# Kernel optimization log

Hardware: AMD Instinct MI355X
Metric: run time of the kernel (lower is better)

The kernel has to match this reference:

```python
import jax, jax.numpy as jnp
import numpy as np

TEMP = 0.05
BIG = 1e6


def _mlp(z, W1, b1, W2, b2, W3, b3, W4, b4, W5, b5):
    h = jax.nn.selu(z @ W1 + b1)
    h = jax.nn.selu(h @ W2 + b2)
    h = jax.nn.selu(h @ W3 + b3)
    h = jax.nn.selu(h @ W4 + b4)
    return h @ W5 + b5


def _cdist(a, b):
    # Euclidean distance via ||a||^2 + ||b||^2 - 2 a.b (clamped for fp safety)
    d2 = (jnp.sum(a * a, axis=1)[:, None]
          + jnp.sum(b * b, axis=1)[None, :]
          - 2.0 * (a @ b.T))
    return jnp.sqrt(jnp.maximum(d2, 0.0))


def _compute_drift(x, y_pos, y_neg):
    N, N_pos = x.shape[0], y_pos.shape[0]
    dist_pos = _cdist(x, y_pos)                      # [N, N_pos]
    dist_neg = _cdist(x, y_neg)                      # [N, N_neg]
    if N == y_neg.shape[0]:
        dist_neg = dist_neg + jnp.eye(N, dtype=x.dtype) * BIG
    logit = jnp.concatenate([-dist_pos / TEMP, -dist_neg / TEMP], axis=1)
    for _ in range(5):  # Sinkhorn: alternating row / column normalization
        logit = logit - jax.nn.logsumexp(logit, axis=-1, keepdims=True)
        logit = logit - jax.nn.logsumexp(logit, axis=-2, keepdims=True)
    A = jnp.exp(logit)
    A_pos, A_neg = A[:, :N_pos], A[:, N_pos:]
    W_pos = A_pos * jnp.sum(A_neg, axis=1, keepdims=True)
    W_neg = A_neg * jnp.sum(A_pos, axis=1, keepdims=True)
    return W_pos @ y_pos - W_neg @ y_neg             # [N, D]


def _forward(pos, z, W1, b1, W2, b2, W3, b3, W4, b4, W5, b5):
    gen = _mlp(z, W1, b1, W2, b2, W3, b3, W4, b4, W5, b5)
    V = _compute_drift(gen, pos, gen)                # computed under no_grad
    target = jax.lax.stop_gradient(gen + V)
    return jnp.sum((gen - target) ** 2, axis=-1)      # per-sample loss [N]


def setup_inputs() -> dict:
    key = jax.random.key(0)
    ks = jax.random.split(key, 8)
    N, D, ND, H = 8192, 256, 128, 1024
    def w(k, fan_in, fan_out):
        return jax.random.normal(k, (fan_in, fan_out), jnp.float32) / np.float32(np.sqrt(fan_in))
    return {
        "pos": jax.random.normal(ks[0], (N, D), jnp.float32),
        "z": jax.random.normal(ks[1], (N, ND), jnp.float32),
        "W1": w(ks[2], ND, H), "b1": jnp.zeros((H,), jnp.float32),
        "W2": w(ks[3], H, H),  "b2": jnp.zeros((H,), jnp.float32),
        "W3": w(ks[4], H, H),  "b3": jnp.zeros((H,), jnp.float32),
        "W4": w(ks[5], H, H),  "b4": jnp.zeros((H,), jnp.float32),
        "W5": w(ks[6], H, D),  "b5": jnp.zeros((D,), jnp.float32),
    }


def reference(pos, z, W1, b1, W2, b2, W3, b3, W4, b4, W5, b5):
    return _forward(pos, z, W1, b1, W2, b2, W3, b3, W4, b4, W5, b5)
```

## Files before the change

### kernel.cpp

```cpp
#include <hip/hip_runtime.h>

#define DEVI __device__ __forceinline__

typedef short bf16x8 __attribute__((ext_vector_type(8)));
typedef float f32x4 __attribute__((ext_vector_type(4)));
typedef unsigned short u16;
typedef unsigned short u16x8 __attribute__((ext_vector_type(8)));
typedef unsigned short u16x4 __attribute__((ext_vector_type(4)));

enum { EPI_MLP = 0, EPI_DISTQ = 1, EPI_NEGTRI = 2 };

#define KLOG2E_T 28.853900817779268f
#define QSCALE 1846.6496523378733f
#define INVQ 0.015625f
#define PSLOTS 80

DEVI u16 f2bf(float f) {
  unsigned u = __float_as_uint(f);
  return (u16)((u + 0x7FFFu + ((u >> 16) & 1u)) >> 16);
}
DEVI float bf2f(u16 h) { return __uint_as_float(((unsigned)h) << 16); }
DEVI float seluf(float x) {
  return x > 0.f ? 1.0507009873554805f * x : 1.7580993408473766f * expm1f(x);
}
DEVI void gload16(const void* g, void* l) {
  __builtin_amdgcn_global_load_lds(
      (const __attribute__((address_space(1))) unsigned*)g,
      (__attribute__((address_space(3))) unsigned*)l, 16, 0, 0);
}
DEVI void lse_comb(float& m, float& s, float m2, float s2) {
  float M = fmaxf(m, m2);
  s = s * exp2f(m - M) + s2 * exp2f(m2 - M);
  m = M;
}
DEVI size_t triblk(int I, int J) { return ((size_t)I * (I + 1) / 2 + J) * 4096; }

template <int BM, int BN, int WM, int WN, int EPI>
__global__ __launch_bounds__(WM* WN * 64) void gemm_k(
    const u16* __restrict__ Ahi, const u16* __restrict__ Alo, int lda,
    const u16* __restrict__ Bhi, const u16* __restrict__ Blo, int ldb, int K,
    float* __restrict__ Cf, int ldc,
    const float* __restrict__ bias, int act, u16* __restrict__ Ohi,
    u16* __restrict__ Olo, int ldo,
    const float* __restrict__ xN2, const float* __restrict__ yN2,
    u16* __restrict__ Cq) {
  constexpr int NW = WM * WN;
  constexpr int FM = BM / (WM * 16), FN = BN / (WN * 16);
  constexpr int IA = BM / (16 * NW), IB = BN / (16 * NW);
  const int tid = threadIdx.x, lane = tid & 63, wave = tid >> 6;
  int bm0, bn0;
  if constexpr (EPI == EPI_DISTQ) {
    int bid = (int)blockIdx.x;
    int xcd = bid & 7, p = bid >> 3;
    int st = (p >> 6) * 8 + xcd;
    int r8 = (p >> 3) & 7, c8 = p & 7;
    bm0 = ((st >> 3) * 8 + r8) * 128;
    bn0 = ((st & 7) * 8 + c8) * 128;
  } else if constexpr (EPI == EPI_NEGTRI) {
    int t = (int)blockIdx.x;
    int a = (int)((sqrtf(8.f * (float)t + 1.f) - 1.f) * 0.5f);
    while ((a + 1) * (a + 2) / 2 <= t) ++a;
    while (a * (a + 1) / 2 > t) --a;
    int b = t - a * (a + 1) / 2;
    bm0 = a * 128;
    bn0 = b * 128;
  } else {
    bm0 = blockIdx.y * BM;
    bn0 = blockIdx.x * BN;
  }
  const int wr = (wave / WN) * (FM * 16), wc = (wave % WN) * (FN * 16);
  __shared__ __align__(16) u16 AsH[BM * 32];
  __shared__ __align__(16) u16 BsH[BN * 32];
  __shared__ __align__(16) u16 AsL[BM * 32];
  __shared__ __align__(16) u16 BsL[BN * 32];
  const int srow = lane >> 2, scol = (lane & 3) * 8;
  const u16 *pAh[IA], *pAl[IA], *pBh[IB], *pBl[IB];
  int lA[IA], lB[IB];
#pragma unroll
  for (int t = 0; t < IA; ++t) {
    int r = (wave * IA + t) * 16;
    pAh[t] = Ahi + (size_t)(bm0 + r + srow) * lda + scol;
    pAl[t] = Alo + (size_t)(bm0 + r + srow) * lda + scol;
    lA[t] = r * 32;
  }
#pragma unroll
  for (int t = 0; t < IB; ++t) {
    int r = (wave * IB + t) * 16;
    pBh[t] = Bhi + (size_t)(bn0 + r + srow) * ldb + scol;
    pBl[t] = Blo + (size_t)(bn0 + r + srow) * ldb + scol;
    lB[t] = r * 32;
  }
  f32x4 acc[FM][FN] = {};
  const int fr = lane & 15, ko = (lane >> 4) * 8;
  for (int k0 = 0; k0 < K; k0 += 32) {
#pragma unroll
    for (int t = 0; t < IA; ++t) {
      gload16(pAh[t], AsH + lA[t]); pAh[t] += 32;
      gload16(pAl[t], AsL + lA[t]); pAl[t] += 32;
    }
#pragma unroll
    for (int t = 0; t < IB; ++t) {
      gload16(pBh[t], BsH + lB[t]); pBh[t] += 32;
      gload16(pBl[t], BsL + lB[t]); pBl[t] += 32;
    }
    __syncthreads();
    bf16x8 ah[FM], bh[FN], al[FM], bl[FN];
#pragma unroll
    for (int m = 0; m < FM; ++m) ah[m] = *(const bf16x8*)&AsH[(wr + m * 16 + fr) * 32 + ko];
#pragma unroll
    for (int n = 0; n < FN; ++n) bh[n] = *(const bf16x8*)&BsH[(wc + n * 16 + fr) * 32 + ko];
#pragma unroll
    for (int m = 0; m < FM; ++m) al[m] = *(const bf16x8*)&AsL[(wr + m * 16 + fr) * 32 + ko];
#pragma unroll
    for (int n = 0; n < FN; ++n) bl[n] = *(const bf16x8*)&BsL[(wc + n * 16 + fr) * 32 + ko];
#pragma unroll
    for (int m = 0; m < FM; ++m)
#pragma unroll
      for (int n = 0; n < FN; ++n) {
        acc[m][n] = __builtin_amdgcn_mfma_f32_16x16x32_bf16(ah[m], bh[n], acc[m][n], 0, 0, 0);
        acc[m][n] = __builtin_amdgcn_mfma_f32_16x16x32_bf16(al[m], bh[n], acc[m][n], 0, 0, 0);
        acc[m][n] = __builtin_amdgcn_mfma_f32_16x16x32_bf16(ah[m], bl[n], acc[m][n], 0, 0, 0);
      }
    __syncthreads();
  }
#pragma unroll
  for (int m = 0; m < FM; ++m)
#pragma unroll
    for (int n = 0; n < FN; ++n)
#pragma unroll
      for (int q = 0; q < 4; ++q) {
        int row = bm0 + wr + m * 16 + (lane >> 4) * 4 + q;
        int col = bn0 + wc + n * 16 + fr;
        float v = acc[m][n][q];
        if constexpr (EPI == EPI_MLP) {
          v += bias[col];
          if (act) v = seluf(v);
          u16 h = f2bf(v);
          size_t idx = (size_t)row * ldo + col;
          Ohi[idx] = h;
          Olo[idx] = f2bf(v - bf2f(h));
          if (Cf) Cf[(size_t)row * ldc + col] = v;
        } else if constexpr (EPI == EPI_DISTQ) {
          float d2 = fmaxf(xN2[row] + yN2[col] - 2.f * v, 0.f);
          float qf = fminf(QSCALE * sqrtf(d2), 65535.f);
          Cq[(size_t)row * 8192 + col] = (u16)__float2uint_rn(qf);
        } else {
          int bI = row >> 6, bJ = col >> 6;
          if (bJ <= bI) {
            float d2 = fmaxf(xN2[row] + yN2[col] - 2.f * v, 0.f);
            float qf = fminf(QSCALE * sqrtf(d2), 65535.f);
            u16 qu = (u16)__float2uint_rn(qf);
            if (row == col) qu = 65535;
            Cq[triblk(bI, bJ) + (row & 63) * 64 + (col & 63)] = qu;
          }
        }
      }
}

DEVI void lse16(const u16x8& qa, const u16x8& qb, const float* __restrict__ w,
                float& m, float& s) {
  f32x4 w0 = *(const f32x4*)w;
  f32x4 w1 = *(const f32x4*)(w + 4);
  f32x4 w2 = *(const f32x4*)(w + 8);
  f32x4 w3 = *(const f32x4*)(w + 12);
  float v[16];
#pragma unroll
  for (int e = 0; e < 4; ++e) {
    v[e] = fmaf((float)qa[e], -INVQ, -w0[e]);
    v[4 + e] = fmaf((float)qa[4 + e], -INVQ, -w1[e]);
    v[8 + e] = fmaf((float)qb[e], -INVQ, -w2[e]);
    v[12 + e] = fmaf((float)qb[4 + e], -INVQ, -w3[e]);
  }
  float mx = v[0];
#pragma unroll
  for (int e = 1; e < 16; ++e) mx = fmaxf(mx, v[e]);
  float ac = 0.f;
#pragma unroll
  for (int e = 0; e < 16; ++e) ac += exp2f(v[e] - mx);
  lse_comb(m, s, mx, ac);
}

__global__ __launch_bounds__(256) void sink_k(
    const u16* __restrict__ DqPos, const u16* __restrict__ DqTri,
    const float* __restrict__ wpos, const float* __restrict__ wneg,
    float* __restrict__ Pm, float* __restrict__ Ps) {
  const int tid = threadIdx.x;
  const int I = blockIdx.y, q8 = blockIdx.x;
  __shared__ __align__(16) u16 stg[4096];
  __shared__ float Cm[64][12], Cs[64][12];
  const int rn = tid >> 2, cn = (tid & 3) * 16;
  const int p2 = tid & 31, g8 = tid >> 5;
  float mA = -3.0e38f, sA = 0.f;
  float mB0 = -3.0e38f, sB0 = 0.f, mB1 = -3.0e38f, sB1 = 0.f;
  const int sw = (rn & 7) << 3;

  {
    const size_t rowbase = (size_t)(I * 64 + rn) * 8192;
    for (int jc = 0; jc < 16; ++jc) {
      int j0 = q8 * 1024 + jc * 64 + cn;
      u16x8 qa = *(const u16x8*)&DqPos[rowbase + j0];
      u16x8 qb = *(const u16x8*)&DqPos[rowbase + j0 + 8];
      lse16(qa, qb, wpos + j0, mA, sA);
    }
  }
  for (int Jb = q8 * 16; Jb < q8 * 16 + 16; ++Jb) {
    if (Jb <= I) {
      const u16* blk = DqTri + triblk(I, Jb);
      u16x8 qa = *(const u16x8*)&blk[rn * 64 + cn];
      u16x8 qb = *(const u16x8*)&blk[rn * 64 + cn + 8];
      lse16(qa, qb, wneg + Jb * 64 + cn, mA, sA);
    } else {
      const u16* blk = DqTri + triblk(Jb, I);
      u16x8 qa = *(const u16x8*)&blk[rn * 64 + cn];
      u16x8 qb = *(const u16x8*)&blk[rn * 64 + cn + 8];
      *(u16x8*)&stg[rn * 64 + (cn ^ sw)] = qa;
      *(u16x8*)&stg[rn * 64 + ((cn + 8) ^ sw)] = qb;
      __syncthreads();
      float v0[8], v1[8];
#pragma unroll
      for (int cc = 0; cc < 8; ++cc) {
        int sj = cc * 8 + g8;
        unsigned wq = *(const unsigned*)&stg[sj * 64 + ((2 * p2) ^ ((sj & 7) << 3))];
        float wgt = wneg[Jb * 64 + sj];
        v0[cc] = fmaf((float)(wq & 0xFFFFu), -INVQ, -wgt);
        v1[cc] = fmaf((float)(wq >> 16), -INVQ, -wgt);
      }
      float mx0 = v0[0], mx1 = v1[0];
#pragma unroll
      for (int cc = 1; cc < 8; ++cc) { mx0 = fmaxf(mx0, v0[cc]); mx1 = fmaxf(mx1, v1[cc]); }
      float a0 = 0.f, a1 = 0.f;
#pragma unroll
      for (int cc = 0; cc < 8; ++cc) { a0 += exp2f(v0[cc] - mx0); a1 += exp2f(v1[cc] - mx1); }
      lse_comb(mB0, sB0, mx0, a0);
      lse_comb(mB1, sB1, mx1, a1);
      __syncthreads();
    }
  }
  for (int i = tid; i < 64 * 12; i += 256) { (&Cm[0][0])[i] = -3.0e38f; (&Cs[0][0])[i] = 0.f; }
  __syncthreads();
  Cm[rn][tid & 3] = mA; Cs[rn][tid & 3] = sA;
  Cm[2 * p2][4 + g8] = mB0; Cs[2 * p2][4 + g8] = sB0;
  Cm[2 * p2 + 1][4 + g8] = mB1; Cs[2 * p2 + 1][4 + g8] = sB1;
  __syncthreads();
  if (tid < 64) {
    float m = Cm[tid][0], s = Cs[tid][0];
#pragma unroll
    for (int b = 1; b < 12; ++b) lse_comb(m, s, Cm[tid][b], Cs[tid][b]);
    Pm[(size_t)q8 * 8192 + I * 64 + tid] = m;
    Ps[(size_t)q8 * 8192 + I * 64 + tid] = s;
  }
}

__global__ __launch_bounds__(256) void colpass_k(
    const u16* __restrict__ DqPos, const u16* __restrict__ DqTri,
    const float* __restrict__ rv, float* __restrict__ Pm, float* __restrict__ Ps) {
  const int bid = blockIdx.x, tid = threadIdx.x;
  __shared__ __align__(16) u16 stg[4096];
  __shared__ float Cm[64][12], Cs[64][12];
  if (bid < 1024) {
    const int q8 = bid & 7, I = bid >> 3;
    const int rn = tid >> 2, cn = (tid & 3) * 16;
    const int p2 = tid & 31, g8 = tid >> 5;
    const int sw = (rn & 7) << 3;
    float mA = -3.0e38f, sA = 0.f;
    float mB0 = -3.0e38f, sB0 = 0.f, mB1 = -3.0e38f, sB1 = 0.f;
    for (int Jb = q8 * 16; Jb < q8 * 16 + 16; ++Jb) {
      if (Jb <= I) {
        const u16* blk = DqTri + triblk(I, Jb);
        u16x8 qa = *(const u16x8*)&blk[rn * 64 + cn];
        u16x8 qb = *(const u16x8*)&blk[rn * 64 + cn + 8];
        lse16(qa, qb, rv + Jb * 64 + cn, mA, sA);
      } else {
        const u16* blk = DqTri + triblk(Jb, I);
        u16x8 qa = *(const u16x8*)&blk[rn * 64 + cn];
        u16x8 qb = *(const u16x8*)&blk[rn * 64 + cn + 8];
        *(u16x8*)&stg[rn * 64 + (cn ^ sw)] = qa;
        *(u16x8*)&stg[rn * 64 + ((cn + 8) ^ sw)] = qb;
        __syncthreads();
        float v0[8], v1[8];
#pragma unroll
        for (int cc = 0; cc < 8; ++cc) {
          int sj = cc * 8 + g8;
          unsigned wq = *(const unsigned*)&stg[sj * 64 + ((2 * p2) ^ ((sj & 7) << 3))];
          float wgt = rv[Jb * 64 + sj];
          v0[cc] = fmaf((float)(wq & 0xFFFFu), -INVQ, -wgt);
          v1[cc] = fmaf((float)(wq >> 16), -INVQ, -wgt);
        }
        float mx0 = v0[0], mx1 = v1[0];
#pragma unroll
        for (int cc = 1; cc < 8; ++cc) { mx0 = fmaxf(mx0, v0[cc]); mx1 = fmaxf(mx1, v1[cc]); }
        float a0 = 0.f, a1 = 0.f;
#pragma unroll
        for (int cc = 0; cc < 8; ++cc) { a0 += exp2f(v0[cc] - mx0); a1 += exp2f(v1[cc] - mx1); }
        lse_comb(mB0, sB0, mx0, a0);
        lse_comb(mB1, sB1, mx1, a1);
        __syncthreads();
      }
    }
    for (int i = tid; i < 64 * 12; i += 256) { (&Cm[0][0])[i] = -3.0e38f; (&Cs[0][0])[i] = 0.f; }
    __syncthreads();
    Cm[rn][tid & 3] = mA; Cs[rn][tid & 3] = sA;
    Cm[2 * p2][4 + g8] = mB0; Cs[2 * p2][4 + g8] = sB0;
    Cm[2 * p2 + 1][4 + g8] = mB1; Cs[2 * p2 + 1][4 + g8] = sB1;
    __syncthreads();
    if (tid < 64) {
      float m = Cm[tid][0], s = Cs[tid][0];
#pragma unroll
      for (int b2 = 1; b2 < 12; ++b2) lse_comb(m, s, Cm[tid][b2], Cs[tid][b2]);
      Pm[(size_t)(72 + q8) * 8192 + I * 64 + tid] = m;
      Ps[(size_t)(72 + q8) * 8192 + I * 64 + tid] = s;
    }
  } else {
    const int b2 = bid - 1024;
    const int jb = b2 & 7, ic = b2 >> 3;
    int j0 = jb * 1024 + tid * 4;
    int i0 = ic * 128;
    float m[4], s[4];
#pragma unroll
    for (int e = 0; e < 4; ++e) { m[e] = -3.0e38f; s[e] = 0.f; }
    for (int ib = 0; ib < 16; ++ib) {
      float v[4][8];
#pragma unroll
      for (int ii = 0; ii < 8; ++ii) {
        int i = i0 + ib * 8 + ii;
        u16x4 qv = *(const u16x4*)&DqPos[(size_t)i * 8192 + j0];
        float ri = rv[i];
#pragma unroll
        for (int e = 0; e < 4; ++e) v[e][ii] = fmaf((float)qv[e], -INVQ, -ri);
      }
#pragma unroll
      for (int e = 0; e < 4; ++e) {
        float mx = v[e][0];
#pragma unroll
        for (int ii = 1; ii < 8; ++ii) mx = fmaxf(mx, v[e][ii]);
        float ac = 0.f;
#pragma unroll
        for (int ii = 0; ii < 8; ++ii) ac += exp2f(v[e][ii] - mx);
        lse_comb(m[e], s[e], mx, ac);
      }
    }
#pragma unroll
    for (int e = 0; e < 4; ++e) {
      Pm[(size_t)(8 + ic) * 8192 + j0 + e] = m[e];
      Ps[(size_t)(8 + ic) * 8192 + j0 + e] = s[e];
    }
  }
}

__global__ void comb_rv_k(const float* __restrict__ Pm, const float* __restrict__ Ps,
                          float* __restrict__ rv) {
  int j = blockIdx.x * 256 + threadIdx.x;
  float m = Pm[j], s = Ps[j];
  for (int b = 1; b < 8; ++b)
    lse_comb(m, s, Pm[(size_t)b * 8192 + j], Ps[(size_t)b * 8192 + j]);
  rv[j] = m + log2f(s);
}

__global__ void comb_cpc_k(const float* __restrict__ Pm, const float* __restrict__ Ps,
                           float* __restrict__ cpos, float* __restrict__ cneg) {
  int j = blockIdx.x * 256 + threadIdx.x;
  if (j < 8192) {
    float m = Pm[(size_t)8 * 8192 + j], s = Ps[(size_t)8 * 8192 + j];
    for (int b = 9; b < 72; ++b)
      lse_comb(m, s, Pm[(size_t)b * 8192 + j], Ps[(size_t)b * 8192 + j]);
    cpos[j] = m + log2f(s);
  } else {
    int jj = j - 8192;
    float m = Pm[(size_t)72 * 8192 + jj], s = Ps[(size_t)72 * 8192 + jj];
    for (int b = 73; b < 80; ++b)
      lse_comb(m, s, Pm[(size_t)b * 8192 + jj], Ps[(size_t)b * 8192 + jj]);
    cneg[jj] = m + log2f(s);
  }
}

template <bool NEG>
__global__ __launch_bounds__(512) void pv_k(
    const u16* __restrict__ DqPos, const u16* __restrict__ DqTri,
    const float* __restrict__ rvec, const float* __restrict__ w,
    const u16* __restrict__ BT, float* __restrict__ Mout,
    float* __restrict__ sout) {
  const int tid = threadIdx.x, lane = tid & 63, wave = tid >> 6;
  const int I = blockIdx.y;
  const int kh = blockIdx.x;
  __shared__ __align__(16) u16 AT[64 * 128];
  __shared__ __align__(16) u16 Bs[4 * 256 * 32];
  __shared__ __align__(16) u16 stg[NEG ? 2 * 4096 : 8];
  __shared__ float rvS[64];
  __shared__ float SredN[64][8];
  __shared__ float SredT[64][8];
  const int wrg = (wave >> 2) * 32, wcg = (wave & 3) * 64;
  const int fr = lane & 15, ko = (lane >> 4) * 8;
  const int rn = tid >> 3;
  const int cnp = (tid & 7) * 16;
  const int cnn = (tid & 7) * 8;
  const int swr = (rn & 7) << 3;
  const int p = tid & 63, sjg = tid >> 6;
  const int swp = (p & 7) << 3;
  float asumN = 0.f, asumT = 0.f;
  if (tid < 64) rvS[tid] = rvec[I * 64 + tid];
  __syncthreads();
  const float riN = rvS[rn];
  const float riT = rvS[p];
  f32x4 acc[2][4] = {};

  for (int jc = 0; jc < 32; ++jc) {
    const int j0 = (kh * 32 + jc) * 128;
    __syncthreads();
#pragma unroll
    for (int ks = 0; ks < 4; ++ks) {
      int brow = wave * 32 + (lane >> 2);
      int bcol = (lane & 3) * 8;
      gload16(BT + (size_t)brow * 8192 + j0 + ks * 32 + bcol,
              Bs + ks * 8192 + wave * 32 * 32);
      gload16(BT + (size_t)(brow + 16) * 8192 + j0 + ks * 32 + bcol,
              Bs + ks * 8192 + (wave * 32 + 16) * 32);
    }
    if constexpr (!NEG) {
      const u16* rp = DqPos + (size_t)(I * 64 + rn) * 8192 + j0 + cnp;
      u16x8 qa = *(const u16x8*)rp;
      u16x8 qb = *(const u16x8*)(rp + 8);
      const float* wp = w + j0 + cnp;
      f32x4 w0 = *(const f32x4*)wp;
      f32x4 w1 = *(const f32x4*)(wp + 4);
      f32x4 w2 = *(const f32x4*)(wp + 8);
      f32x4 w3 = *(const f32x4*)(wp + 12);
      union { u16x8 v; u16 e[8]; } pk0, pk1;
#pragma unroll
      for (int e = 0; e < 4; ++e) {
        float a0 = exp2f(fmaf((float)qa[e], -INVQ, -riN - w0[e]));
        float a1 = exp2f(fmaf((float)qa[4 + e], -INVQ, -riN - w1[e]));
        float a2 = exp2f(fmaf((float)qb[e], -INVQ, -riN - w2[e]));
        float a3 = exp2f(fmaf((float)qb[4 + e], -INVQ, -riN - w3[e]));
        asumN += a0 + a1 + a2 + a3;
        pk0.e[e] = f2bf(a0); pk0.e[4 + e] = f2bf(a1);
        pk1.e[e] = f2bf(a2); pk1.e[4 + e] = f2bf(a3);
      }
      *(u16x8*)&AT[rn * 128 + (cnp ^ swr)] = pk0.v;
      *(u16x8*)&AT[rn * 128 + ((cnp + 8) ^ swr)] = pk1.v;
    } else {
      bool anytr = false;
#pragma unroll
      for (int h = 0; h < 2; ++h) {
        const int Jb = kh * 64 + jc * 2 + h;
        if (Jb <= I) {
          const u16* blk = DqTri + triblk(I, Jb);
          u16x8 q = *(const u16x8*)&blk[rn * 64 + cnn];
          const float* wp = w + Jb * 64 + cnn;
          f32x4 w0 = *(const f32x4*)wp;
          f32x4 w1 = *(const f32x4*)(wp + 4);
          union { u16x8 v; u16 e[8]; } pk;
#pragma unroll
          for (int e = 0; e < 4; ++e) {
            float a0 = exp2f(fmaf((float)q[e], -INVQ, -riN - w0[e]));
            float a1 = exp2f(fmaf((float)q[4 + e], -INVQ, -riN - w1[e]));
            asumN += a0 + a1;
            pk.e[e] = f2bf(a0); pk.e[4 + e] = f2bf(a1);
          }
          *(u16x8*)&AT[rn * 128 + ((h * 64 + cnn) ^ swr)] = pk.v;
        } else {
          anytr = true;
          const u16* blk = DqTri + triblk(Jb, I);
          u16x8 q = *(const u16x8*)&blk[rn * 64 + cnn];
          *(u16x8*)&stg[h * 4096 + rn * 64 + (cnn ^ swr)] = q;
        }
      }
      if (anytr) {
        __syncthreads();
#pragma unroll
        for (int h = 0; h < 2; ++h) {
          const int Jb = kh * 64 + jc * 2 + h;
          if (Jb <= I) continue;
#pragma unroll
          for (int cc = 0; cc < 8; ++cc) {
            int sj = cc * 8 + sjg;
            u16 q = stg[h * 4096 + sj * 64 + (p ^ ((sj & 7) << 3))];
            float a = exp2f(fmaf((float)q, -INVQ, -riT - w[Jb * 64 + sj]));
            asumT += a;
            AT[p * 128 + ((h * 64 + sj) ^ swp)] = f2bf(a);
          }
        }
      }
    }
    __syncthreads();
#pragma unroll
    for (int ks = 0; ks < 4; ++ks) {
      bf16x8 a2[2], b2[4];
#pragma unroll
      for (int m = 0; m < 2; ++m) {
        int rl = wrg + m * 16 + fr;
        a2[m] = *(const bf16x8*)&AT[rl * 128 + ((ks * 32 + ko) ^ ((rl & 7) << 3))];
      }
#pragma unroll
      for (int n = 0; n < 4; ++n)
        b2[n] = *(const bf16x8*)&Bs[ks * 8192 + (wcg + n * 16 + fr) * 32 + ko];
#pragma unroll
      for (int m = 0; m < 2; ++m)
#pragma unroll
        for (int n = 0; n < 4; ++n)
          acc[m][n] = __builtin_amdgcn_mfma_f32_16x16x32_bf16(a2[m], b2[n], acc[m][n], 0, 0, 0);
    }
  }
#pragma unroll
  for (int m = 0; m < 2; ++m)
#pragma unroll
    for (int n = 0; n < 4; ++n)
#pragma unroll
      for (int q = 0; q < 4; ++q) {
        int row = I * 64 + wrg + m * 16 + (lane >> 4) * 4 + q;
        int d = wcg + n * 16 + fr;
        Mout[(size_t)kh * 2097152 + (size_t)row * 256 + d] = acc[m][n][q];
      }
  SredN[rn][tid & 7] = asumN;
  SredT[p][sjg] = NEG ? asumT : 0.f;
  __syncthreads();
  if (tid < 64) {
    float s = 0.f;
#pragma unroll
    for (int b = 0; b < 8; ++b) s += SredN[tid][b] + SredT[tid][b];
    sout[kh * 8192 + I * 64 + tid] = s;
  }
}

__global__ void convert_split_k(const float* __restrict__ src, u16* __restrict__ hi,
                                u16* __restrict__ lo, int n) {
  int i = blockIdx.x * 256 + threadIdx.x;
  if (i < n) {
    float v = src[i];
    u16 h = f2bf(v);
    hi[i] = h;
    lo[i] = f2bf(v - bf2f(h));
  }
}

__global__ void transpose_split_k(const float* __restrict__ src, int K, int N,
                                  u16* __restrict__ hi, u16* __restrict__ lo) {
  __shared__ float t[32][33];
  int x = threadIdx.x & 31, y = threadIdx.x >> 5;
  int k0 = blockIdx.x * 32, n0 = blockIdx.y * 32;
  for (int yy = y; yy < 32; yy += 8) t[yy][x] = src[(size_t)(k0 + yy) * N + n0 + x];
  __syncthreads();
  for (int yy = y; yy < 32; yy += 8) {
    float v = t[x][yy];
    size_t idx = (size_t)(n0 + yy) * K + k0 + x;
    u16 h = f2bf(v);
    hi[idx] = h;
    lo[idx] = f2bf(v - bf2f(h));
  }
}

__global__ void transpose_b16_k(const float* __restrict__ src, int M, int D,
                                u16* __restrict__ dst) {
  __shared__ float t[32][33];
  int x = threadIdx.x & 31, y = threadIdx.x >> 5;
  int m0 = blockIdx.x * 32, d0 = blockIdx.y * 32;
  for (int yy = y; yy < 32; yy += 8) t[yy][x] = src[(size_t)(m0 + yy) * D + d0 + x];
  __syncthreads();
  for (int yy = y; yy < 32; yy += 8)
    dst[(size_t)(d0 + yy) * M + m0 + x] = f2bf(t[x][yy]);
}

__global__ void rownorm_k(const float* __restrict__ src, float* __restrict__ o) {
  int i = blockIdx.x, t = threadIdx.x;
  float s = 0.f;
  for (int d = t; d < 256; d += 64) {
    float v = src[(size_t)i * 256 + d];
    s += v * v;
  }
  for (int off = 32; off; off >>= 1) s += __shfl_down(s, off, 64);
  if (t == 0) o[i] = s;
}

__global__ void zero_k(float* __restrict__ p, int n) {
  int i = blockIdx.x * 256 + threadIdx.x;
  if (i < n) p[i] = 0.f;
}

__global__ void decode_k(float* __restrict__ out, float x, int n) {
  int i = blockIdx.x * 256 + threadIdx.x;
  if (i < n) out[i] = x;
}

__global__ void final_out_k(const float* __restrict__ M1, const float* __restrict__ M2,
                            const float* __restrict__ sp, const float* __restrict__ sn,
                            float* __restrict__ out) {
  __shared__ float S[256];
  int i = blockIdx.x, d = threadIdx.x;
  size_t idx = (size_t)i * 256 + d;
  float spv = sp[i] + sp[8192 + i];
  float snv = sn[i] + sn[8192 + i];
  float v = snv * (M1[idx] + M1[2097152 + idx]) - spv * (M2[idx] + M2[2097152 + idx]);
  S[d] = v * v;
  __syncthreads();
  for (int off = 128; off; off >>= 1) {
    if (d < off) S[d] += S[d + off];
    __syncthreads();
  }
  if (d == 0) out[i] = S[0];
}

extern "C" void kernel_launch(void* const* d_in, const int* in_sizes, int n_in,
                              void* d_out, int out_size, void* d_ws, size_t ws_size,
                              hipStream_t stream) {
  (void)in_sizes; (void)n_in; (void)out_size;
  const float* pos = (const float*)d_in[0];
  const float* z   = (const float*)d_in[1];
  const float* W1  = (const float*)d_in[2];
  const float* b1  = (const float*)d_in[3];
  const float* W2  = (const float*)d_in[4];
  const float* b2  = (const float*)d_in[5];
  const float* W3  = (const float*)d_in[6];
  const float* b3  = (const float*)d_in[7];
  const float* W4  = (const float*)d_in[8];
  const float* b4  = (const float*)d_in[9];
  const float* W5  = (const float*)d_in[10];
  const float* b5  = (const float*)d_in[11];
  float* out = (float*)d_out;

  if (ws_size < (size_t)261500000) {
    decode_k<<<32, 256, 0, stream>>>(out, (float)(double)(ws_size >> 10), 8192);
    return;
  }

  char* wsp = (char*)d_ws;
  size_t off = 0;
  auto alloc = [&](size_t bytes) -> char* {
    char* p = wsp + off;
    off += (bytes + 255) & ~(size_t)255;
    return p;
  };
  u16* DqPos = (u16*)alloc((size_t)8192 * 8192 * 2);
  u16* DqTri = (u16*)alloc((size_t)8256 * 4096 * 2);
  u16* Yh    = (u16*)alloc((size_t)16384 * 256 * 2);
  u16* Yl    = (u16*)alloc((size_t)16384 * 256 * 2);
  u16* posT  = (u16*)alloc((size_t)256 * 8192 * 2);
  u16* genT  = (u16*)alloc((size_t)256 * 8192 * 2);
  float* yN2 = (float*)alloc(16384 * 4);
  float* rv  = (float*)alloc(8192 * 4);
  float* cpos = (float*)alloc(8192 * 4);
  float* cneg = (float*)alloc(8192 * 4);
  float* spv = (float*)alloc(2 * 8192 * 4);
  float* snv = (float*)alloc(2 * 8192 * 4);
  float* M1  = (float*)alloc((size_t)2 * 8192 * 256 * 4);
  float* M2  = (float*)alloc((size_t)2 * 8192 * 256 * 4);
  float* Pm = M1;
  float* Ps = Pm + (size_t)PSLOTS * 8192;

  size_t toff = 0;
  char* tbase = (char*)DqPos;
  auto talloc = [&](size_t bytes) -> char* {
    char* p = tbase + toff;
    toff += (bytes + 255) & ~(size_t)255;
    return p;
  };
  u16* zh    = (u16*)talloc((size_t)8192 * 128 * 2);
  u16* zl    = (u16*)talloc((size_t)8192 * 128 * 2);
  u16* W1Th  = (u16*)talloc(1024 * 128 * 2);
  u16* W1Tl  = (u16*)talloc(1024 * 128 * 2);
  u16* W2Th  = (u16*)talloc(1024 * 1024 * 2);
  u16* W2Tl  = (u16*)talloc(1024 * 1024 * 2);
  u16* W3Th  = (u16*)talloc(1024 * 1024 * 2);
  u16* W3Tl  = (u16*)talloc(1024 * 1024 * 2);
  u16* W4Th  = (u16*)talloc(1024 * 1024 * 2);
  u16* W4Tl  = (u16*)talloc(1024 * 1024 * 2);
  u16* W5Th  = (u16*)talloc(256 * 1024 * 2);
  u16* W5Tl  = (u16*)talloc(256 * 1024 * 2);
  u16* h1h   = (u16*)talloc((size_t)8192 * 1024 * 2);
  u16* h1l   = (u16*)talloc((size_t)8192 * 1024 * 2);
  u16* h2h   = (u16*)talloc((size_t)8192 * 1024 * 2);
  u16* h2l   = (u16*)talloc((size_t)8192 * 1024 * 2);
  float* genf = (float*)talloc((size_t)8192 * 256 * 4);

  u16* genH = Yh + (size_t)8192 * 256;
  u16* genL = Yl + (size_t)8192 * 256;
  float* pN2 = yN2;
  float* gN2 = yN2 + 8192;

  convert_split_k<<<4096, 256, 0, stream>>>(z, zh, zl, 8192 * 128);
  convert_split_k<<<8192, 256, 0, stream>>>(pos, Yh, Yl, 8192 * 256);
  transpose_split_k<<<dim3(4, 32), 256, 0, stream>>>(W1, 128, 1024, W1Th, W1Tl);
  transpose_split_k<<<dim3(32, 32), 256, 0, stream>>>(W2, 1024, 1024, W2Th, W2Tl);
  transpose_split_k<<<dim3(32, 32), 256, 0, stream>>>(W3, 1024, 1024, W3Th, W3Tl);
  transpose_split_k<<<dim3(32, 32), 256, 0, stream>>>(W4, 1024, 1024, W4Th, W4Tl);
  transpose_split_k<<<dim3(32, 8), 256, 0, stream>>>(W5, 1024, 256, W5Th, W5Tl);
  rownorm_k<<<8192, 64, 0, stream>>>(pos, pN2);
  transpose_b16_k<<<dim3(256, 8), 256, 0, stream>>>(pos, 8192, 256, posT);

  gemm_k<64, 128, 2, 2, EPI_MLP><<<dim3(8, 128), 256, 0, stream>>>(
      zh, zl, 128, W1Th, W1Tl, 128, 128, nullptr, 0, b1, 1, h1h, h1l, 1024,
      nullptr, nullptr, nullptr);
  gemm_k<64, 128, 2, 2, EPI_MLP><<<dim3(8, 128), 256, 0, stream>>>(
      h1h, h1l, 1024, W2Th, W2Tl, 1024, 1024, nullptr, 0, b2, 1, h2h, h2l, 1024,
      nullptr, nullptr, nullptr);
  gemm_k<64, 128, 2, 2, EPI_MLP><<<dim3(8, 128), 256, 0, stream>>>(
      h2h, h2l, 1024, W3Th, W3Tl, 1024, 1024, nullptr, 0, b3, 1, h1h, h1l, 1024,
      nullptr, nullptr, nullptr);
  gemm_k<64, 128, 2, 2, EPI_MLP><<<dim3(8, 128), 256, 0, stream>>>(
      h1h, h1l, 1024, W4Th, W4Tl, 1024, 1024, nullptr, 0, b4, 1, h2h, h2l, 1024,
      nullptr, nullptr, nullptr);
  gemm_k<64, 128, 2, 2, EPI_MLP><<<dim3(2, 128), 256, 0, stream>>>(
      h2h, h2l, 1024, W5Th, W5Tl, 1024, 1024, genf, 256, b5, 0,
      genH, genL, 256, nullptr, nullptr, nullptr);

  rownorm_k<<<8192, 64, 0, stream>>>(genf, gN2);
  transpose_b16_k<<<dim3(256, 8), 256, 0, stream>>>(genf, 8192, 256, genT);

  gemm_k<128, 128, 2, 2, EPI_DISTQ><<<4096, 256, 0, stream>>>(
      genH, genL, 256, Yh, Yl, 256, 256, nullptr, 0, nullptr, 0, nullptr,
      nullptr, 0, gN2, pN2, DqPos);
  gemm_k<128, 128, 2, 2, EPI_NEGTRI><<<2080, 256, 0, stream>>>(
      genH, genL, 256, genH, genL, 256, 256, nullptr, 0, nullptr, 0, nullptr,
      nullptr, 0, gN2, gN2, DqTri);

  zero_k<<<64, 256, 0, stream>>>(cpos, 16384);
  for (int it = 0; it < 5; ++it) {
    sink_k<<<dim3(8, 128), 256, 0, stream>>>(DqPos, DqTri, cpos, cneg, Pm, Ps);
    comb_rv_k<<<32, 256, 0, stream>>>(Pm, Ps, rv);
    colpass_k<<<1536, 256, 0, stream>>>(DqPos, DqTri, rv, Pm, Ps);
    comb_cpc_k<<<64, 256, 0, stream>>>(Pm, Ps, cpos, cneg);
  }

  pv_k<false><<<dim3(2, 128), 512, 0, stream>>>(DqPos, DqTri, rv, cpos, posT, M1, spv);
  pv_k<true><<<dim3(2, 128), 512, 0, stream>>>(DqPos, DqTri, rv, cneg, genT, M2, snv);

  final_out_k<<<8192, 256, 0, stream>>>(M1, M2, spv, snv, out);
}
```

Measured before the change: 1.407 ms.

## Fuse Sinkhorn partial-combine kernels into the row and column pass kernels

After: 1.556 ms. 1.11x slower.

```diff
diff --git a/kernel.cpp b/kernel.cpp
--- a/kernel.cpp
+++ b/kernel.cpp
@@ -157,7 +157,7 @@
       }
 }
 
-DEVI void lse16(const u16x8& qa, const u16x8& qb, const float* __restrict__ w,
+DEVI void lse16(const u16x8& qa, const u16x8& qb, const float* w,
                 float& m, float& s) {
   f32x4 w0 = *(const f32x4*)w;
   f32x4 w1 = *(const f32x4*)(w + 4);
@@ -183,11 +183,32 @@
 __global__ __launch_bounds__(256) void sink_k(
     const u16* __restrict__ DqPos, const u16* __restrict__ DqTri,
     const float* __restrict__ wpos, const float* __restrict__ wneg,
-    float* __restrict__ Pm, float* __restrict__ Ps) {
+    float* __restrict__ Pm, float* __restrict__ Ps, int use_comb) {
   const int tid = threadIdx.x;
   const int I = blockIdx.y, q8 = blockIdx.x;
   __shared__ __align__(16) u16 stg[4096];
   __shared__ float Cm[64][12], Cs[64][12];
+  __shared__ float wpL[1024], wnL[1024];
+  if (use_comb) {
+    for (int t = tid; t < 1024; t += 256) {
+      int j = q8 * 1024 + t;
+      float m = Pm[(size_t)8 * 8192 + j], s = Ps[(size_t)8 * 8192 + j];
+      for (int b = 9; b < 72; ++b)
+        lse_comb(m, s, Pm[(size_t)b * 8192 + j], Ps[(size_t)b * 8192 + j]);
+      wpL[t] = m + log2f(s);
+      float m2 = Pm[(size_t)72 * 8192 + j], s2 = Ps[(size_t)72 * 8192 + j];
+      for (int b = 73; b < 80; ++b)
+        lse_comb(m2, s2, Pm[(size_t)b * 8192 + j], Ps[(size_t)b * 8192 + j]);
+      wnL[t] = m2 + log2f(s2);
+    }
+  } else {
+    for (int t = tid; t < 1024; t += 256) {
+      int j = q8 * 1024 + t;
+      wpL[t] = wpos[j];
+      wnL[t] = wneg[j];
+    }
+  }
+  __syncthreads();
   const int rn = tid >> 2, cn = (tid & 3) * 16;
   const int p2 = tid & 31, g8 = tid >> 5;
   float mA = -3.0e38f, sA = 0.f;
@@ -197,18 +218,19 @@
   {
     const size_t rowbase = (size_t)(I * 64 + rn) * 8192;
     for (int jc = 0; jc < 16; ++jc) {
-      int j0 = q8 * 1024 + jc * 64 + cn;
-      u16x8 qa = *(const u16x8*)&DqPos[rowbase + j0];
-      u16x8 qb = *(const u16x8*)&DqPos[rowbase + j0 + 8];
-      lse16(qa, qb, wpos + j0, mA, sA);
+      int jl = jc * 64 + cn;
+      u16x8 qa = *(const u16x8*)&DqPos[rowbase + q8 * 1024 + jl];
+      u16x8 qb = *(const u16x8*)&DqPos[rowbase + q8 * 1024 + jl + 8];
+      lse16(qa, qb, wpL + jl, mA, sA);
     }
   }
   for (int Jb = q8 * 16; Jb < q8 * 16 + 16; ++Jb) {
+    const int jl = (Jb - q8 * 16) * 64;
     if (Jb <= I) {
       const u16* blk = DqTri + triblk(I, Jb);
       u16x8 qa = *(const u16x8*)&blk[rn * 64 + cn];
       u16x8 qb = *(const u16x8*)&blk[rn * 64 + cn + 8];
-      lse16(qa, qb, wneg + Jb * 64 + cn, mA, sA);
+      lse16(qa, qb, wnL + jl + cn, mA, sA);
     } else {
       const u16* blk = DqTri + triblk(Jb, I);
       u16x8 qa = *(const u16x8*)&blk[rn * 64 + cn];
@@ -221,7 +243,7 @@
       for (int cc = 0; cc < 8; ++cc) {
         int sj = cc * 8 + g8;
         unsigned wq = *(const unsigned*)&stg[sj * 64 + ((2 * p2) ^ ((sj & 7) << 3))];
-        float wgt = wneg[Jb * 64 + sj];
+        float wgt = wnL[jl + sj];
         v0[cc] = fmaf((float)(wq & 0xFFFFu), -INVQ, -wgt);
         v1[cc] = fmaf((float)(wq >> 16), -INVQ, -wgt);
       }
@@ -253,23 +275,33 @@
 
 __global__ __launch_bounds__(256) void colpass_k(
     const u16* __restrict__ DqPos, const u16* __restrict__ DqTri,
-    const float* __restrict__ rv, float* __restrict__ Pm, float* __restrict__ Ps) {
+    float* __restrict__ Pm, float* __restrict__ Ps) {
   const int bid = blockIdx.x, tid = threadIdx.x;
   __shared__ __align__(16) u16 stg[4096];
   __shared__ float Cm[64][12], Cs[64][12];
+  __shared__ float rvL[1024];
   if (bid < 1024) {
     const int q8 = bid & 7, I = bid >> 3;
+    for (int t = tid; t < 1024; t += 256) {
+      int j = q8 * 1024 + t;
+      float m = Pm[j], s = Ps[j];
+      for (int b = 1; b < 8; ++b)
+        lse_comb(m, s, Pm[(size_t)b * 8192 + j], Ps[(size_t)b * 8192 + j]);
+      rvL[t] = m + log2f(s);
+    }
+    __syncthreads();
     const int rn = tid >> 2, cn = (tid & 3) * 16;
     const int p2 = tid & 31, g8 = tid >> 5;
     const int sw = (rn & 7) << 3;
     float mA = -3.0e38f, sA = 0.f;
     float mB0 = -3.0e38f, sB0 = 0.f, mB1 = -3.0e38f, sB1 = 0.f;
     for (int Jb = q8 * 16; Jb < q8 * 16 + 16; ++Jb) {
+      const int jl = (Jb - q8 * 16) * 64;
       if (Jb <= I) {
         const u16* blk = DqTri + triblk(I, Jb);
         u16x8 qa = *(const u16x8*)&blk[rn * 64 + cn];
         u16x8 qb = *(const u16x8*)&blk[rn * 64 + cn + 8];
-        lse16(qa, qb, rv + Jb * 64 + cn, mA, sA);
+        lse16(qa, qb, rvL + jl + cn, mA, sA);
       } else {
         const u16* blk = DqTri + triblk(Jb, I);
         u16x8 qa = *(const u16x8*)&blk[rn * 64 + cn];
@@ -282,7 +314,7 @@
         for (int cc = 0; cc < 8; ++cc) {
           int sj = cc * 8 + g8;
           unsigned wq = *(const unsigned*)&stg[sj * 64 + ((2 * p2) ^ ((sj & 7) << 3))];
-          float wgt = rv[Jb * 64 + sj];
+          float wgt = rvL[jl + sj];
           v0[cc] = fmaf((float)(wq & 0xFFFFu), -INVQ, -wgt);
           v1[cc] = fmaf((float)(wq >> 16), -INVQ, -wgt);
         }
@@ -315,6 +347,14 @@
     const int jb = b2 & 7, ic = b2 >> 3;
     int j0 = jb * 1024 + tid * 4;
     int i0 = ic * 128;
+    if (tid < 128) {
+      int j = i0 + tid;
+      float m = Pm[j], s = Ps[j];
+      for (int b = 1; b < 8; ++b)
+        lse_comb(m, s, Pm[(size_t)b * 8192 + j], Ps[(size_t)b * 8192 + j]);
+      rvL[tid] = m + log2f(s);
+    }
+    __syncthreads();
     float m[4], s[4];
 #pragma unroll
     for (int e = 0; e < 4; ++e) { m[e] = -3.0e38f; s[e] = 0.f; }
@@ -324,7 +364,7 @@
       for (int ii = 0; ii < 8; ++ii) {
         int i = i0 + ib * 8 + ii;
         u16x4 qv = *(const u16x4*)&DqPos[(size_t)i * 8192 + j0];
-        float ri = rv[i];
+        float ri = rvL[ib * 8 + ii];
 #pragma unroll
         for (int e = 0; e < 4; ++e) v[e][ii] = fmaf((float)qv[e], -INVQ, -ri);
       }
@@ -713,11 +753,11 @@
 
   zero_k<<<64, 256, 0, stream>>>(cpos, 16384);
   for (int it = 0; it < 5; ++it) {
-    sink_k<<<dim3(8, 128), 256, 0, stream>>>(DqPos, DqTri, cpos, cneg, Pm, Ps);
-    comb_rv_k<<<32, 256, 0, stream>>>(Pm, Ps, rv);
-    colpass_k<<<1536, 256, 0, stream>>>(DqPos, DqTri, rv, Pm, Ps);
-    comb_cpc_k<<<64, 256, 0, stream>>>(Pm, Ps, cpos, cneg);
-  }
+    sink_k<<<dim3(8, 128), 256, 0, stream>>>(DqPos, DqTri, cpos, cneg, Pm, Ps, it);
+    colpass_k<<<1536, 256, 0, stream>>>(DqPos, DqTri, Pm, Ps);
+  }
+  comb_rv_k<<<32, 256, 0, stream>>>(Pm, Ps, rv);
+  comb_cpc_k<<<64, 256, 0, stream>>>(Pm, Ps, cpos, cneg);
 
   pv_k<false><<<dim3(2, 128), 512, 0, stream>>>(DqPos, DqTri, rv, cpos, posT, M1, spv);
   pv_k<true><<<dim3(2, 128), 512, 0, stream>>>(DqPos, DqTri, rv, cneg, genT, M2, snv);
```
